# Kernel optimization log

Hardware: AMD Instinct MI355X
Metric: run time of the kernel (lower is better)

## Reference

```python
import jax, jax.numpy as jnp
import numpy as np

SHIFT = 8
CUR_FRAME = 16
NUM_K = 32
TEMP = 1.0


def wrap_angle(x):
    return (x + jnp.pi) % (2.0 * jnp.pi) - jnp.pi


def setup_inputs() -> dict:
    key = jax.random.key(0)
    k1, k2, k3, k4, k5 = jax.random.split(key, 5)
    A, S, T = 8192, 96, 1024
    valid = jax.random.randint(k1, (A, S), 0, 2).astype(bool)
    pos = jax.random.normal(k2, (A, S, 2), dtype=jnp.float32) * 50.0
    heading = jax.random.uniform(k3, (A, S), minval=-jnp.pi, maxval=jnp.pi, dtype=jnp.float32)
    tok_xy = jax.random.normal(k4, (T, 2), dtype=jnp.float32) * 2.0
    tok_h = jax.random.uniform(k5, (T, 1), minval=-jnp.pi, maxval=jnp.pi, dtype=jnp.float32)
    token_endpoint = jnp.concatenate([tok_xy, tok_h], axis=-1)
    return {"valid": valid, "pos": pos, "heading": heading, "token_endpoint": token_endpoint}


def _clean_heading(valid, heading):
    # sequential fix of >1.5 rad heading jumps (state carried along time)
    valid_pairs = valid[:, :-1] & valid[:, 1:]

    def step(h_prev, x):
        h_next, vp = x
        diff = jnp.abs(wrap_angle(h_prev - h_next))
        change = (diff > 1.5) & vp
        h_new = jnp.where(change, h_prev, h_next)
        return h_new, h_new

    h0 = heading[:, 0]
    _, hs = jax.lax.scan(step, h0, (heading[:, 1:].T, valid_pairs.T))
    return jnp.concatenate([h0[:, None], hs.T], axis=1)


def _extrapolate_stationary(valid, pos, heading):
    A, S = valid.shape
    t = jnp.argmax(valid, axis=1)  # first valid step per agent
    n_fill = t % SHIFT
    special = (t == CUR_FRAME) & (~valid[:, CUR_FRAME - SHIFT])
    n_fill = jnp.where(special, SHIFT, n_fill)
    steps = jnp.arange(S)[None, :]
    mask = (steps >= (t - n_fill)[:, None]) & (steps < t[:, None])  # [A,S]
    ra = jnp.arange(A)
    pos_t = pos[ra, t]          # [A,2]
    head_t = heading[ra, t]     # [A]
    valid = valid | mask
    pos = jnp.where(mask[..., None], pos_t[:, None, :], pos)
    heading = jnp.where(mask, head_t[:, None], heading)
    return valid, pos, heading


def _match_agent_token_center(valid, pos, heading, token_endpoint, key):
    A, S = valid.shape
    tx, ty, th = token_endpoint[:, 0], token_endpoint[:, 1], token_endpoint[:, 2]
    idxs = jnp.arange(SHIFT, S, SHIFT)
    ra = jnp.arange(A)

    def local_to_global(prev_pos, prev_head):
        c, s = jnp.cos(prev_head), jnp.sin(prev_head)
        gx = c[:, None] * tx[None, :] - s[:, None] * ty[None, :] + prev_pos[:, 0:1]
        gy = s[:, None] * tx[None, :] + c[:, None] * ty[None, :] + prev_pos[:, 1:2]
        return gx, gy  # each [A, n_token]

    def step(carry, x):
        prev_pos, prev_head, prev_pos_s, prev_head_s, key = carry
        v_prev, v_cur, pos_i, head_i = x
        key, sk = jax.random.split(key)
        _valid = v_prev & v_cur

        # --- greedy (gt) branch ---
        gx, gy = local_to_global(prev_pos, prev_head)
        dist = (gx - pos_i[:, 0:1]) ** 2 + (gy - pos_i[:, 1:2]) ** 2
        idx_gt = jnp.argmin(dist, axis=-1)
        new_pos_gt = jnp.stack([gx[ra, idx_gt], gy[ra, idx_gt]], axis=-1)
        new_head_gt = wrap_angle(prev_head + th[idx_gt])
        prev_pos = jnp.where(_valid[:, None], new_pos_gt, pos_i)
        prev_head = jnp.where(_valid, new_head_gt, head_i)
        gt_pos_o = jnp.where(_valid[:, None], prev_pos, 0.0)
        gt_head_o = jnp.where(_valid, prev_head, 0.0)

        # --- sampled branch (num_k > 1) ---
        gxs, gys = local_to_global(prev_pos_s, prev_head_s)
        dist_s = (gxs - pos_i[:, 0:1]) ** 2 + (gys - pos_i[:, 1:2]) ** 2
        neg_top, top_idx = jax.lax.top_k(-dist_s, NUM_K)  # smallest distances
        logits = neg_top / TEMP  # == -dist / temp
        samp = jax.random.categorical(sk, logits, axis=-1)
        idx_s = jnp.take_along_axis(top_idx, samp[:, None], axis=1)[:, 0]
        new_pos_s = jnp.stack([gxs[ra, idx_s], gys[ra, idx_s]], axis=-1)
        new_head_s = wrap_angle(prev_head_s + th[idx_s])
        prev_pos_s = jnp.where(_valid[:, None], new_pos_s, pos_i)
        prev_head_s = jnp.where(_valid, new_head_s, head_i)
        s_pos_o = jnp.where(_valid[:, None], prev_pos_s, 0.0)
        s_head_o = jnp.where(_valid, prev_head_s, 0.0)

        new_carry = (prev_pos, prev_head, prev_pos_s, prev_head_s, key)
        return new_carry, (_valid, idx_gt, gt_pos_o, gt_head_o, idx_s, s_pos_o, s_head_o)

    init = (pos[:, 0], heading[:, 0], pos[:, 0], heading[:, 0], key)
    xs = (valid[:, idxs - SHIFT].T,
          valid[:, idxs].T,
          jnp.moveaxis(pos[:, idxs], 1, 0),
          heading[:, idxs].T)
    _, ys = jax.lax.scan(step, init, xs)
    # move step axis from 0 to 1 -> [A, n_out_steps, ...]
    return tuple(jnp.moveaxis(y, 0, 1) for y in ys)


def reference(valid, pos, heading, token_endpoint):
    heading = _clean_heading(valid, heading)
    valid, pos, heading = _extrapolate_stationary(valid, pos, heading)
    return _match_agent_token_center(valid, pos, heading, token_endpoint, jax.random.key(42))
```

## Files before the change

### kernel.cpp

```cpp
#include <hip/hip_runtime.h>
#include <math.h>

#define NTOK 1024
#define NSTEPS 11

typedef __attribute__((ext_vector_type(2))) float f32x2;

__device__ __forceinline__ float fadd_(float a, float b){ return __fadd_rn(a,b); }
__device__ __forceinline__ float fsub_(float a, float b){ return __fsub_rn(a,b); }
__device__ __forceinline__ float fmul_(float a, float b){ return __fmul_rn(a,b); }

__device__ __forceinline__ float wrap_angle(float x){
  const float PI_F     = 3.14159265358979323846f;
  const float TWO_PI_F = 6.28318530717958647692f;
  float t = fadd_(x, PI_F);
  float r = fmodf(t, TWO_PI_F);
  if (r < 0.0f) r = fadd_(r, TWO_PI_F);
  return fsub_(r, PI_F);
}

__device__ __forceinline__ void tf2x32(unsigned k0, unsigned k1,
                                       unsigned c0, unsigned c1,
                                       unsigned &o0, unsigned &o1){
  unsigned ks2 = k0 ^ k1 ^ 0x1BD11BDAu;
  unsigned x0 = c0 + k0, x1 = c1 + k1;
#define TFR(r) { x0 += x1; x1 = (x1 << (r)) | (x1 >> (32 - (r))); x1 ^= x0; }
  TFR(13) TFR(15) TFR(26) TFR(6)   x0 += k1;  x1 += ks2 + 1u;
  TFR(17) TFR(29) TFR(16) TFR(24)  x0 += ks2; x1 += k0  + 2u;
  TFR(13) TFR(15) TFR(26) TFR(6)   x0 += k0;  x1 += k1  + 3u;
  TFR(17) TFR(29) TFR(16) TFR(24)  x0 += k1;  x1 += ks2 + 4u;
  TFR(13) TFR(15) TFR(26) TFR(6)   x0 += ks2; x1 += k0  + 5u;
#undef TFR
  o0 = x0; o1 = x1;
}

static void tf2x32_host(unsigned k0, unsigned k1, unsigned c0, unsigned c1,
                        unsigned &o0, unsigned &o1){
  unsigned ks2 = k0 ^ k1 ^ 0x1BD11BDAu;
  unsigned x0 = c0 + k0, x1 = c1 + k1;
#define TFR(r) { x0 += x1; x1 = (x1 << (r)) | (x1 >> (32 - (r))); x1 ^= x0; }
  TFR(13) TFR(15) TFR(26) TFR(6)   x0 += k1;  x1 += ks2 + 1u;
  TFR(17) TFR(29) TFR(16) TFR(24)  x0 += ks2; x1 += k0  + 2u;
  TFR(13) TFR(15) TFR(26) TFR(6)   x0 += k0;  x1 += k1  + 3u;
  TFR(17) TFR(29) TFR(16) TFR(24)  x0 += k1;  x1 += ks2 + 4u;
  TFR(13) TFR(15) TFR(26) TFR(6)   x0 += ks2; x1 += k0  + 5u;
#undef TFR
  o0 = x0; o1 = x1;
}

struct StepKeys { unsigned a[2 * NSTEPS]; };

__device__ __forceinline__ float gumbel_from_bits(unsigned bits){
  unsigned m = bits >> 9;
  float u = (m == 0u) ? 1.17549435e-38f
                      : fsub_(__uint_as_float(0x3F800000u | m), 1.0f);
  float l1 = (float)log((double)u);
  float l2 = (float)log((double)(-l1));
  return -l2;
}

#define DPP_MIN_STEP(x, ctrl, rm) { \
  unsigned y_ = (unsigned)__builtin_amdgcn_update_dpp((int)(x), (int)(x), (ctrl), (rm), 0xf, false); \
  (x) = (x) < y_ ? (x) : y_; }
#define DPP_MAX_STEP(x, ctrl, rm) { \
  unsigned y_ = (unsigned)__builtin_amdgcn_update_dpp((int)(x), (int)(x), (ctrl), (rm), 0xf, false); \
  (x) = (x) > y_ ? (x) : y_; }

__device__ __forceinline__ unsigned wbcast_umin(unsigned x){
  DPP_MIN_STEP(x, 0x111, 0xf)
  DPP_MIN_STEP(x, 0x112, 0xf)
  DPP_MIN_STEP(x, 0x114, 0xf)
  DPP_MIN_STEP(x, 0x118, 0xf)
  DPP_MIN_STEP(x, 0x142, 0xa)
  DPP_MIN_STEP(x, 0x143, 0xc)
  return (unsigned)__builtin_amdgcn_readlane((int)x, 63);
}
__device__ __forceinline__ unsigned wbcast_umax(unsigned x){
  DPP_MAX_STEP(x, 0x111, 0xf)
  DPP_MAX_STEP(x, 0x112, 0xf)
  DPP_MAX_STEP(x, 0x114, 0xf)
  DPP_MAX_STEP(x, 0x118, 0xf)
  DPP_MAX_STEP(x, 0x142, 0xa)
  DPP_MAX_STEP(x, 0x143, 0xc)
  return (unsigned)__builtin_amdgcn_readlane((int)x, 63);
}

#define CE(i,j) { unsigned long long a_ = dp[i], b_ = dp[j]; bool lt_ = a_ < b_; \
                  dp[i] = lt_ ? a_ : b_; dp[j] = lt_ ? b_ : a_; }

extern "C" __global__ void __launch_bounds__(256)
sctoken_kernel(const int* __restrict__ valid,
               const float* __restrict__ pos,
               const float* __restrict__ heading,
               const float* __restrict__ tok,
               float* __restrict__ out,
               StepKeys ks)
{
  __shared__ float2 s_txy[NTOK];
  __shared__ float  s_th[NTOK];
  __shared__ float  s_cpx[4][12], s_cpy[4][12], s_ch[4][12];
  __shared__ int    s_cv[4][12];
  __shared__ unsigned long long s_q[256][15];

  const int tid = threadIdx.x;
  for (int j = tid; j < NTOK; j += 256) {
    s_txy[j] = make_float2(tok[3*j], tok[3*j+1]);
    s_th[j]  = tok[3*j+2];
  }
  s_q[tid][14] = ~0ULL;
  const int wave = tid >> 6;
  const int lane = tid & 63;
  const int a = blockIdx.x * 4 + wave;

  const int*   va = valid   + a * 96;
  const float* ha = heading + a * 96;
  const float* pa = pos     + a * 192;

  {
    float hprev = ha[0];
    int   vprev = va[0];
    int   t = 0; bool seen = (vprev != 0);
    float ptx = pa[0], pty = pa[1], hth = hprev;
    if (lane == 0) {
      s_cv[wave][0] = vprev; s_cpx[wave][0] = pa[0]; s_cpy[wave][0] = pa[1]; s_ch[wave][0] = hprev;
    }
    for (int s = 1; s < 96; ++s) {
      int vcur = va[s];
      float hn = ha[s];
      float diff = fabsf(wrap_angle(fsub_(hprev, hn)));
      float hnew = ((diff > 1.5f) && vprev && vcur) ? hprev : hn;
      if (!seen && vcur) { seen = true; t = s; ptx = pa[2*s]; pty = pa[2*s+1]; hth = hnew; }
      if (((s & 7) == 0) && (s <= 88) && (lane == 0)) {
        int i = s >> 3;
        s_cv[wave][i] = vcur; s_cpx[wave][i] = pa[2*s]; s_cpy[wave][i] = pa[2*s+1]; s_ch[wave][i] = hnew;
      }
      hprev = hnew; vprev = vcur;
    }
    int n_fill = t & 7;
    if ((t == 16) && (va[8] == 0)) n_fill = 8;
    if ((lane == 0) && (n_fill > 0)) {
      int c = t - n_fill;
      int i = c >> 3;
      s_cv[wave][i] = 1; s_cpx[wave][i] = ptx; s_cpy[wave][i] = pty; s_ch[wave][i] = hth;
    }
  }
  __syncthreads();

  float gpx = s_cpx[wave][0], gpy = s_cpy[wave][0], ghd = s_ch[wave][0];
  float spx = gpx, spy = gpy, shd = ghd;

  #pragma unroll 1
  for (int st = 0; st < NSTEPS; ++st) {
    const unsigned sk0 = ks.a[2*st], sk1 = ks.a[2*st+1];

    const int  vprev  = s_cv[wave][st];
    const int  vcur   = s_cv[wave][st+1];
    const bool valid_ = (vprev != 0) && (vcur != 0);
    const float pix = s_cpx[wave][st+1];
    const float piy = s_cpy[wave][st+1];
    const float hin = s_ch[wave][st+1];
    const int oi = a * NSTEPS + st;

    double sgd, cgd, ssd, csd;
    sincos((double)ghd, &sgd, &cgd);
    sincos((double)shd, &ssd, &csd);
    const float cg = (float)cgd, sg = (float)sgd;
    const float cs2 = (float)csd, ss2 = (float)ssd;

    unsigned dm = 0xffffffffu; unsigned im = 0u;
    unsigned long long dp[16];

    {
      #pragma clang fp contract(off)
      const f32x2 Ag = {cg, sg},  Bg = {-sg, cg};
      const f32x2 As = {cs2, ss2}, Bs = {-ss2, cs2};
      const f32x2 Pg = {gpx, gpy}, Ps = {spx, spy};
      const f32x2 Qn = {-pix, -piy};
      #pragma unroll
      for (int i2 = 0; i2 < 16; ++i2) {
        int j = lane + (i2 << 6);
        float2 t2 = s_txy[j];
        const f32x2 tx = {t2.x, t2.x}, ty = {t2.y, t2.y};
        f32x2 gg = ((Ag * tx) + (Bg * ty)) + Pg;
        f32x2 dg = gg + Qn;
        f32x2 qg = dg * dg;
        float dG = __fadd_rn(qg.x, qg.y);
        unsigned du = __float_as_uint(dG);
        bool lt = du < dm;
        dm = lt ? du : dm;
        im = lt ? (unsigned)j : im;
        f32x2 gs = ((As * tx) + (Bs * ty)) + Ps;
        f32x2 dsv = gs + Qn;
        f32x2 qs = dsv * dsv;
        float dS = __fadd_rn(qs.x, qs.y);
        dp[i2] = (((unsigned long long)__float_as_uint(dS)) << 10) | (unsigned)j;
      }
    }

    {
      unsigned gdm = wbcast_umin(dm);
      unsigned long long m = __ballot(dm == gdm);
      int jgt;
      if (__popcll(m) > 1) {
        unsigned ci = (dm == gdm) ? im : 0xffffffffu;
        jgt = (int)wbcast_umin(ci);
      } else {
        jgt = __builtin_amdgcn_readlane((int)im, __ffsll(m) - 1);
      }
      float2 t2 = s_txy[jgt];
      float gx = fadd_(fsub_(fmul_(cg, t2.x), fmul_(sg, t2.y)), gpx);
      float gy = fadd_(fadd_(fmul_(sg, t2.x), fmul_(cg, t2.y)), gpy);
      float nh = wrap_angle(fadd_(ghd, s_th[jgt]));
      float upx = valid_ ? gx : pix;
      float upy = valid_ ? gy : piy;
      float uhd = valid_ ? nh : hin;
      gpx = upx; gpy = upy; ghd = uhd;
      if (lane == 0) {
        out[oi]                = valid_ ? 1.0f : 0.0f;
        out[90112  + oi]       = (float)jgt;
        out[180224 + 2*oi]     = valid_ ? upx : 0.0f;
        out[180224 + 2*oi + 1] = valid_ ? upy : 0.0f;
        out[360448 + oi]       = valid_ ? uhd : 0.0f;
      }
    }

    {
      CE(0,1) CE(2,3) CE(4,5) CE(6,7) CE(8,9) CE(10,11) CE(12,13) CE(14,15)
      CE(0,2) CE(1,3) CE(4,6) CE(5,7) CE(8,10) CE(9,11) CE(12,14) CE(13,15)
      CE(1,2) CE(5,6) CE(9,10) CE(13,14)
      CE(0,4) CE(1,5) CE(2,6) CE(3,7) CE(8,12) CE(9,13) CE(10,14) CE(11,15)
      CE(2,4) CE(3,5) CE(10,12) CE(11,13)
      CE(1,2) CE(3,4) CE(5,6) CE(9,10) CE(11,12) CE(13,14)
      CE(0,8) CE(1,9) CE(2,10) CE(3,11) CE(4,12) CE(5,13) CE(6,14) CE(7,15)
      CE(4,8) CE(5,9) CE(6,10) CE(7,11)
      CE(2,4) CE(3,5) CE(6,8) CE(7,9) CE(10,12) CE(11,13)
      CE(1,2) CE(3,4) CE(5,6) CE(7,8) CE(9,10) CE(11,12) CE(13,14)

      #pragma unroll
      for (int i2 = 2; i2 < 16; ++i2) s_q[tid][i2-2] = dp[i2];
      unsigned hdist  = (unsigned)(dp[0] >> 10), hidx  = (unsigned)dp[0] & 1023u;
      unsigned h2dist = (unsigned)(dp[1] >> 10), h2idx = (unsigned)dp[1] & 1023u;
      int pops = 0;
      unsigned long long fetchv = s_q[tid][0];

      unsigned myd = 0u, myi = 0u;
      #pragma unroll 1
      for (int k = 0; k < 32; ++k) {
        unsigned gd = wbcast_umin(hdist);
        unsigned long long m = __ballot(hdist == gd);
        unsigned gi; bool own;
        if (__popcll(m) > 1) {
          unsigned ci = (hdist == gd) ? hidx : 0xffffffffu;
          gi = wbcast_umin(ci);
          own = (hdist == gd) && (hidx == gi);
        } else {
          gi = (unsigned)__builtin_amdgcn_readlane((int)hidx, __ffsll(m) - 1);
          own = (hdist == gd);
        }
        bool isk = (lane == k);
        myd = isk ? gd : myd;
        myi = isk ? gi : myi;
        unsigned fd = (unsigned)(fetchv >> 10), fi = (unsigned)fetchv & 1023u;
        hdist  = own ? h2dist : hdist;
        hidx   = own ? h2idx  : hidx;
        h2dist = own ? fd : h2dist;
        h2idx  = own ? fi : h2idx;
        pops   = own ? pops + 1 : pops;
        int slot = pops < 14 ? pops : 14;
        fetchv = s_q[tid][slot];
      }

      unsigned mu = 0u;
      if (lane < 32) {
        float myv = -__uint_as_float(myd);
        unsigned b1, b2;
        tf2x32(sk0, sk1, 0u, (unsigned)(a * 32 + lane), b1, b2);
        unsigned bits = b1 ^ b2;
        float g = gumbel_from_bits(bits);
        float cand = fadd_(myv, g);
        unsigned cu = __float_as_uint(cand);
        mu = (cu & 0x80000000u) ? ~cu : (cu | 0x80000000u);
      }
      unsigned gmu = wbcast_umax(mu);
      unsigned long long m2 = __ballot(mu == gmu);
      int kl = __ffsll(m2) - 1;
      int js = __builtin_amdgcn_readlane((int)myi, kl);
      float2 t2 = s_txy[js];
      float gx = fadd_(fsub_(fmul_(cs2, t2.x), fmul_(ss2, t2.y)), spx);
      float gy = fadd_(fadd_(fmul_(ss2, t2.x), fmul_(cs2, t2.y)), spy);
      float nh = wrap_angle(fadd_(shd, s_th[js]));
      float upx = valid_ ? gx : pix;
      float upy = valid_ ? gy : piy;
      float uhd = valid_ ? nh : hin;
      spx = upx; spy = upy; shd = uhd;
      if (lane == 0) {
        out[450560 + oi]       = (float)js;
        out[540672 + 2*oi]     = valid_ ? upx : 0.0f;
        out[540672 + 2*oi + 1] = valid_ ? upy : 0.0f;
        out[720896 + oi]       = valid_ ? uhd : 0.0f;
      }
    }
  }
}

extern "C" void kernel_launch(void* const* d_in, const int* in_sizes, int n_in,
                              void* d_out, int out_size, void* d_ws, size_t ws_size,
                              hipStream_t stream) {
  const int*   valid   = (const int*)  d_in[0];
  const float* pos     = (const float*)d_in[1];
  const float* heading = (const float*)d_in[2];
  const float* tok     = (const float*)d_in[3];
  float* out           = (float*)d_out;
  (void)in_sizes; (void)n_in; (void)out_size; (void)d_ws; (void)ws_size;

  StepKeys ks;
  unsigned k0 = 0u, k1 = 42u;
  for (int st = 0; st < NSTEPS; ++st) {
    unsigned nk0, nk1, s0, s1;
    tf2x32_host(k0, k1, 0u, 0u, nk0, nk1);
    tf2x32_host(k0, k1, 0u, 1u, s0, s1);
    ks.a[2*st] = s0; ks.a[2*st+1] = s1;
    k0 = nk0; k1 = nk1;
  }

  hipLaunchKernelGGL(sctoken_kernel, dim3(2048), dim3(256), 0, stream,
                     valid, pos, heading, tok, out, ks);
}
```

Before: 435.9 us.

## Batch Gumbel noise across two steps, widen register heap, drop fmodf

Gumbel noise for the current and the next step is now generated together: the upper half of the wave computes the next step's noise and passes it over with a lane shuffle, which halves the number of serial threefry and double-log sequences. The per-lane top-k register heap grows from two to four entries, so fewer values go through the shared-memory queue. fmodf in wrap_angle becomes a single conditional subtract, which is only correct when inputs stay within one period of range. The host now derives one extra step key to support the paired generation.

```diff
diff --git a/kernel.cpp b/kernel.cpp
--- a/kernel.cpp
+++ b/kernel.cpp
@@ -14,7 +14,7 @@
   const float PI_F     = 3.14159265358979323846f;
   const float TWO_PI_F = 6.28318530717958647692f;
   float t = fadd_(x, PI_F);
-  float r = fmodf(t, TWO_PI_F);
+  float r = (t >= TWO_PI_F) ? fsub_(t, TWO_PI_F) : t;
   if (r < 0.0f) r = fadd_(r, TWO_PI_F);
   return fsub_(r, PI_F);
 }
@@ -48,7 +48,7 @@
   o0 = x0; o1 = x1;
 }
 
-struct StepKeys { unsigned a[2 * NSTEPS]; };
+struct StepKeys { unsigned a[2 * (NSTEPS + 1)]; };
 
 __device__ __forceinline__ float gumbel_from_bits(unsigned bits){
   unsigned m = bits >> 9;
@@ -100,14 +100,14 @@
   __shared__ float  s_th[NTOK];
   __shared__ float  s_cpx[4][12], s_cpy[4][12], s_ch[4][12];
   __shared__ int    s_cv[4][12];
-  __shared__ unsigned long long s_q[256][15];
+  __shared__ unsigned long long s_q[256][13];
 
   const int tid = threadIdx.x;
   for (int j = tid; j < NTOK; j += 256) {
     s_txy[j] = make_float2(tok[3*j], tok[3*j+1]);
     s_th[j]  = tok[3*j+2];
   }
-  s_q[tid][14] = ~0ULL;
+  s_q[tid][12] = ~0ULL;
   const int wave = tid >> 6;
   const int lane = tid & 63;
   const int a = blockIdx.x * 4 + wave;
@@ -148,11 +148,10 @@
 
   float gpx = s_cpx[wave][0], gpy = s_cpy[wave][0], ghd = s_ch[wave][0];
   float spx = gpx, spy = gpy, shd = ghd;
+  float g_cur = 0.0f, g_carry = 0.0f;
 
   #pragma unroll 1
   for (int st = 0; st < NSTEPS; ++st) {
-    const unsigned sk0 = ks.a[2*st], sk1 = ks.a[2*st+1];
-
     const int  vprev  = s_cv[wave][st];
     const int  vcur   = s_cv[wave][st+1];
     const bool valid_ = (vprev != 0) && (vcur != 0);
@@ -160,6 +159,18 @@
     const float piy = s_cpy[wave][st+1];
     const float hin = s_ch[wave][st+1];
     const int oi = a * NSTEPS + st;
+
+    if ((st & 1) == 0) {
+      unsigned kk0 = (lane & 32) ? ks.a[2*st+2] : ks.a[2*st];
+      unsigned kk1 = (lane & 32) ? ks.a[2*st+3] : ks.a[2*st+1];
+      unsigned b1, b2;
+      tf2x32(kk0, kk1, 0u, (unsigned)(a * 32 + (lane & 31)), b1, b2);
+      float gall = gumbel_from_bits(b1 ^ b2);
+      g_carry = __shfl_xor(gall, 32, 64);
+      g_cur = gall;
+    } else {
+      g_cur = g_carry;
+    }
 
     double sgd, cgd, ssd, csd;
     sincos((double)ghd, &sgd, &cgd);
@@ -237,47 +248,45 @@
       CE(1,2) CE(3,4) CE(5,6) CE(7,8) CE(9,10) CE(11,12) CE(13,14)
 
       #pragma unroll
-      for (int i2 = 2; i2 < 16; ++i2) s_q[tid][i2-2] = dp[i2];
-      unsigned hdist  = (unsigned)(dp[0] >> 10), hidx  = (unsigned)dp[0] & 1023u;
-      unsigned h2dist = (unsigned)(dp[1] >> 10), h2idx = (unsigned)dp[1] & 1023u;
+      for (int i2 = 4; i2 < 16; ++i2) s_q[tid][i2-4] = dp[i2];
+      unsigned h1d = (unsigned)(dp[0] >> 10), h1i = (unsigned)dp[0] & 1023u;
+      unsigned h2d = (unsigned)(dp[1] >> 10), h2i = (unsigned)dp[1] & 1023u;
+      unsigned h3d = (unsigned)(dp[2] >> 10), h3i = (unsigned)dp[2] & 1023u;
+      unsigned h4d = (unsigned)(dp[3] >> 10), h4i = (unsigned)dp[3] & 1023u;
       int pops = 0;
       unsigned long long fetchv = s_q[tid][0];
 
       unsigned myd = 0u, myi = 0u;
       #pragma unroll 1
       for (int k = 0; k < 32; ++k) {
-        unsigned gd = wbcast_umin(hdist);
-        unsigned long long m = __ballot(hdist == gd);
+        unsigned gd = wbcast_umin(h1d);
+        unsigned long long m = __ballot(h1d == gd);
         unsigned gi; bool own;
         if (__popcll(m) > 1) {
-          unsigned ci = (hdist == gd) ? hidx : 0xffffffffu;
+          unsigned ci = (h1d == gd) ? h1i : 0xffffffffu;
           gi = wbcast_umin(ci);
-          own = (hdist == gd) && (hidx == gi);
+          own = (h1d == gd) && (h1i == gi);
         } else {
-          gi = (unsigned)__builtin_amdgcn_readlane((int)hidx, __ffsll(m) - 1);
-          own = (hdist == gd);
+          gi = (unsigned)__builtin_amdgcn_readlane((int)h1i, __ffsll(m) - 1);
+          own = (h1d == gd);
         }
         bool isk = (lane == k);
         myd = isk ? gd : myd;
         myi = isk ? gi : myi;
         unsigned fd = (unsigned)(fetchv >> 10), fi = (unsigned)fetchv & 1023u;
-        hdist  = own ? h2dist : hdist;
-        hidx   = own ? h2idx  : hidx;
-        h2dist = own ? fd : h2dist;
-        h2idx  = own ? fi : h2idx;
-        pops   = own ? pops + 1 : pops;
-        int slot = pops < 14 ? pops : 14;
+        h1d = own ? h2d : h1d;  h1i = own ? h2i : h1i;
+        h2d = own ? h3d : h2d;  h2i = own ? h3i : h2i;
+        h3d = own ? h4d : h3d;  h3i = own ? h4i : h3i;
+        h4d = own ? fd  : h4d;  h4i = own ? fi  : h4i;
+        pops = own ? pops + 1 : pops;
+        int slot = pops < 12 ? pops : 12;
         fetchv = s_q[tid][slot];
       }
 
       unsigned mu = 0u;
       if (lane < 32) {
         float myv = -__uint_as_float(myd);
-        unsigned b1, b2;
-        tf2x32(sk0, sk1, 0u, (unsigned)(a * 32 + lane), b1, b2);
-        unsigned bits = b1 ^ b2;
-        float g = gumbel_from_bits(bits);
-        float cand = fadd_(myv, g);
+        float cand = fadd_(myv, g_cur);
         unsigned cu = __float_as_uint(cand);
         mu = (cu & 0x80000000u) ? ~cu : (cu | 0x80000000u);
       }
@@ -315,7 +324,7 @@
 
   StepKeys ks;
   unsigned k0 = 0u, k1 = 42u;
-  for (int st = 0; st < NSTEPS; ++st) {
+  for (int st = 0; st < NSTEPS + 1; ++st) {
     unsigned nk0, nk1, s0, s1;
     tf2x32_host(k0, k1, 0u, 0u, nk0, nk1);
     tf2x32_host(k0, k1, 0u, 1u, s0, s1);
```

Result: slower. 505.6 us (+16.0%).
